# Kernel optimization log

Measured on AMD Instinct MI355X. Metric: run time of the kernel, lower is better.

## Reference

```python
import jax, jax.numpy as jnp
import numpy as np

N_NODES = 100000
N_EDGES = 1600000
F_IN, F_HID, F_OUT = 256, 128, 32


def setup_inputs() -> dict:
    key = jax.random.key(0)
    k1, k2, k3, k4 = jax.random.split(key, 4)
    x = jax.random.normal(k1, (N_NODES, F_IN), dtype=jnp.float32)
    edge_index = jax.random.randint(k2, (2, N_EDGES), 0, N_NODES, dtype=jnp.int64)
    W1 = jax.random.normal(k3, (F_IN, F_HID), dtype=jnp.float32) * (1.0 / np.sqrt(F_IN))
    b1 = jnp.zeros((F_HID,), dtype=jnp.float32)
    W2 = jax.random.normal(k4, (F_HID, F_OUT), dtype=jnp.float32) * (1.0 / np.sqrt(F_HID))
    b2 = jnp.zeros((F_OUT,), dtype=jnp.float32)
    return {"x": x, "edge_index": edge_index, "W1": W1, "b1": b1, "W2": W2, "b2": b2}


def _gcn_norm(edge_index, num_nodes):
    # Add self-loops, then symmetric normalization deg^-1/2[src] * deg^-1/2[dst].
    loops = jnp.arange(num_nodes, dtype=edge_index.dtype)
    src = jnp.concatenate([edge_index[0], loops])
    dst = jnp.concatenate([edge_index[1], loops])
    deg = jax.ops.segment_sum(jnp.ones_like(dst, dtype=jnp.float32), dst,
                              num_segments=num_nodes)
    dinv = jnp.where(deg > 0, jax.lax.rsqrt(deg), 0.0)
    norm = dinv[src] * dinv[dst]  # [E + N]
    return src, dst, norm


def _gcn_conv(h, src, dst, norm, num_nodes):
    # h already linearly transformed. Gather sources, scale, scatter-add to dst.
    msgs = h[src] * norm[:, None]
    return jax.ops.segment_sum(msgs, dst, num_segments=num_nodes)


def reference(x, edge_index, W1, b1, W2, b2):
    n = x.shape[0]
    src, dst, norm = _gcn_norm(edge_index, n)
    # Layer 1: linear -> normalized scatter-add -> bias -> relu
    h = _gcn_conv(x @ W1, src, dst, norm, n) + b1
    h = jax.nn.relu(h)
    # F.dropout with training=False (eval mode) is identity.
    # Layer 2
    out = _gcn_conv(h @ W2, src, dst, norm, n) + b2
    return jax.nn.log_softmax(out, axis=1)
```

## Files before the change

### kernel.cpp

```cpp
#include <hip/hip_runtime.h>

#define N_NODES 100000
#define N_EDGES 1600000
#define F_IN 256
#define F_HID 128
#define F_OUT 32
#define NBUCK 391
#define BIN_BLOCKS 512
#define EDGES_PER_BIN 3125

typedef unsigned short ushort_t;
typedef unsigned int uint_t;

using short8  = __attribute__((ext_vector_type(8))) short;
using floatx4 = __attribute__((ext_vector_type(4))) float;

__device__ __forceinline__ ushort_t f2bf(float f) {
    uint_t u = __float_as_uint(f);
    u += 0x7fff + ((u >> 16) & 1);
    return (ushort_t)(u >> 16);
}
__device__ __forceinline__ float bf_lo(uint_t u) { return __uint_as_float(u << 16); }
__device__ __forceinline__ float bf_hi(uint_t u) { return __uint_as_float(u & 0xffff0000u); }

__global__ __launch_bounds__(256) void hist_kernel(const int* __restrict__ ei,
                                                   int* __restrict__ bucket_cnt) {
    __shared__ int h[NBUCK];
    for (int i = threadIdx.x; i < NBUCK; i += 256) h[i] = 0;
    __syncthreads();
    int gid = blockIdx.x * 256 + threadIdx.x;
    for (int e = gid; e < N_EDGES; e += BIN_BLOCKS * 256)
        atomicAdd(&h[ei[N_EDGES + e] >> 8], 1);
    __syncthreads();
    for (int i = threadIdx.x; i < NBUCK; i += 256) {
        int c = h[i];
        if (c) atomicAdd(&bucket_cnt[i], c);
    }
}

__global__ __launch_bounds__(512) void scan_kernel(const int* __restrict__ bucket_cnt,
                                                   int* __restrict__ bucket_base,
                                                   int* __restrict__ bucket_cursor,
                                                   int* __restrict__ offs) {
    __shared__ int s[512];
    int t = threadIdx.x;
    int own = (t < NBUCK) ? bucket_cnt[t] : 0;
    s[t] = own;
    __syncthreads();
    for (int off = 1; off < 512; off <<= 1) {
        int v = (t >= off) ? s[t - off] : 0;
        __syncthreads();
        s[t] += v;
        __syncthreads();
    }
    if (t < NBUCK) {
        int ex = s[t] - own;
        bucket_base[t] = ex;
        bucket_cursor[t] = ex;
    }
    if (t == 0) {
        bucket_base[NBUCK] = N_EDGES;
        offs[N_NODES] = N_EDGES;
    }
}

__global__ __launch_bounds__(256) void bin_kernel(const int* __restrict__ ei,
                                                  int* __restrict__ bucket_cursor,
                                                  int2* __restrict__ binned) {
    __shared__ int h[NBUCK];
    __shared__ int base[NBUCK];
    const int t = threadIdx.x;
    const int beg = blockIdx.x * EDGES_PER_BIN;
    const int end = beg + EDGES_PER_BIN;
    for (int i = t; i < NBUCK; i += 256) h[i] = 0;
    __syncthreads();
    for (int e = beg + t; e < end; e += 256) atomicAdd(&h[ei[N_EDGES + e] >> 8], 1);
    __syncthreads();
    for (int i = t; i < NBUCK; i += 256) {
        int c = h[i];
        base[i] = c ? atomicAdd(&bucket_cursor[i], c) : 0;
        h[i] = 0;
    }
    __syncthreads();
    for (int e = beg + t; e < end; e += 256) {
        int s = ei[e], d = ei[N_EDGES + e];
        int bk = d >> 8;
        int p = base[bk] + atomicAdd(&h[bk], 1);
        binned[p] = make_int2(s, d);
    }
}

__global__ __launch_bounds__(256) void build_kernel(const int2* __restrict__ binned,
                                                    const int* __restrict__ bucket_base,
                                                    int* __restrict__ offs,
                                                    int* __restrict__ csr,
                                                    float* __restrict__ dinv) {
    __shared__ int h[256];
    __shared__ int sc[256];
    __shared__ int cur[256];
    const int b = blockIdx.x, t = threadIdx.x;
    const int beg = bucket_base[b];
    const int end = bucket_base[b + 1];
    h[t] = 0;
    __syncthreads();
    for (int j = beg + t; j < end; j += 256) {
        int2 p = binned[j];
        atomicAdd(&h[p.y & 255], 1);
    }
    __syncthreads();
    int deg = h[t];
    sc[t] = deg;
    __syncthreads();
    for (int off = 1; off < 256; off <<= 1) {
        int v = (t >= off) ? sc[t - off] : 0;
        __syncthreads();
        sc[t] += v;
        __syncthreads();
    }
    int excl = sc[t] - deg;
    cur[t] = excl;
    int node = b * 256 + t;
    if (node < N_NODES) {
        offs[node] = beg + excl;
        dinv[node] = rsqrtf((float)deg + 1.0f);
    }
    __syncthreads();
    for (int j = beg + t; j < end; j += 256) {
        int2 p = binned[j];
        int pos = atomicAdd(&cur[p.y & 255], 1);
        csr[beg + pos] = p.x;
    }
}

__global__ __launch_bounds__(256) void w1t_kernel(const float* __restrict__ W1,
                                                  ushort_t* __restrict__ W1T) {
    int t = blockIdx.x * 256 + threadIdx.x;
#pragma unroll
    for (int j = 0; j < 4; j++) {
        int e = j * 8192 + t;
        int n = e >> 8, k = e & 255;
        W1T[e] = f2bf(W1[k * F_HID + n]);
    }
}

__global__ __launch_bounds__(256) void gemm1_kernel(const float* __restrict__ x,
                                                    const ushort_t* __restrict__ W1T,
                                                    ushort_t* __restrict__ h0bf) {
    __shared__ ushort_t Bst[F_HID][F_IN + 8];
    const int tid = threadIdx.x;
    const int rbase = blockIdx.x * 64;
    const int w = tid >> 6;
    const int lane = tid & 63;
    const int q = lane >> 4;
    const int nloc = lane & 15;

#pragma unroll
    for (int j = 0; j < 16; j++) {
        int f = j * 256 + tid;
        int n = f >> 5, kg = f & 31;
        uint4 v = ((const uint4*)(W1T + n * F_IN))[kg];
        *(uint4*)(&Bst[n][kg * 8]) = v;
    }
    __syncthreads();

    const int rowA = rbase + w * 16 + nloc;
    const bool okA = rowA < N_NODES;
    const float* ap = x + (size_t)rowA * F_IN + q * 8;

    floatx4 acc[8];
#pragma unroll
    for (int t = 0; t < 8; t++) acc[t] = (floatx4){0.f, 0.f, 0.f, 0.f};

#pragma unroll
    for (int k0 = 0; k0 < F_IN; k0 += 32) {
        float4 f0 = make_float4(0.f, 0.f, 0.f, 0.f);
        float4 f1 = make_float4(0.f, 0.f, 0.f, 0.f);
        if (okA) {
            f0 = *(const float4*)(ap + k0);
            f1 = *(const float4*)(ap + k0 + 4);
        }
        short8 a;
        a[0] = (short)f2bf(f0.x); a[1] = (short)f2bf(f0.y);
        a[2] = (short)f2bf(f0.z); a[3] = (short)f2bf(f0.w);
        a[4] = (short)f2bf(f1.x); a[5] = (short)f2bf(f1.y);
        a[6] = (short)f2bf(f1.z); a[7] = (short)f2bf(f1.w);
#pragma unroll
        for (int t = 0; t < 8; t++) {
            short8 b = *(const short8*)(&Bst[t * 16 + nloc][k0 + q * 8]);
            acc[t] = __builtin_amdgcn_mfma_f32_16x16x32_bf16(a, b, acc[t], 0, 0, 0);
        }
    }

#pragma unroll
    for (int reg = 0; reg < 4; reg++) {
        int rowD = rbase + w * 16 + q * 4 + reg;
        if (rowD < N_NODES) {
            ushort_t* op = h0bf + (size_t)rowD * F_HID + nloc;
#pragma unroll
            for (int t = 0; t < 8; t++) op[t * 16] = f2bf(acc[t][reg]);
        }
    }
}

__global__ __launch_bounds__(256) void gather128(const ushort_t* __restrict__ h0bf,
                                                 const int* __restrict__ offs,
                                                 const int* __restrict__ csr,
                                                 const float* __restrict__ dinv,
                                                 ushort_t* __restrict__ aggbf) {
    int node = blockIdx.x * 8 + (threadIdx.x >> 5);
    int l = threadIdx.x & 31;
    float dn = dinv[node];
    uint2 sv = ((const uint2*)(h0bf + (size_t)node * F_HID))[l];
    float s = dn * dn;
    float4 acc;
    acc.x = bf_lo(sv.x) * s; acc.y = bf_hi(sv.x) * s;
    acc.z = bf_lo(sv.y) * s; acc.w = bf_hi(sv.y) * s;

    int beg = offs[node], end = offs[node + 1];
    int j = beg;
    for (; j + 1 < end; j += 2) {
        int s0 = csr[j], s1 = csr[j + 1];
        float n0 = dinv[s0] * dn, n1 = dinv[s1] * dn;
        uint2 v0 = ((const uint2*)(h0bf + (size_t)s0 * F_HID))[l];
        uint2 v1 = ((const uint2*)(h0bf + (size_t)s1 * F_HID))[l];
        acc.x += bf_lo(v0.x) * n0 + bf_lo(v1.x) * n1;
        acc.y += bf_hi(v0.x) * n0 + bf_hi(v1.x) * n1;
        acc.z += bf_lo(v0.y) * n0 + bf_lo(v1.y) * n1;
        acc.w += bf_hi(v0.y) * n0 + bf_hi(v1.y) * n1;
    }
    if (j < end) {
        int s0 = csr[j];
        float n0 = dinv[s0] * dn;
        uint2 v0 = ((const uint2*)(h0bf + (size_t)s0 * F_HID))[l];
        acc.x += bf_lo(v0.x) * n0; acc.y += bf_hi(v0.x) * n0;
        acc.z += bf_lo(v0.y) * n0; acc.w += bf_hi(v0.y) * n0;
    }
    uint2 p;
    p.x = (uint_t)f2bf(acc.x) | ((uint_t)f2bf(acc.y) << 16);
    p.y = (uint_t)f2bf(acc.z) | ((uint_t)f2bf(acc.w) << 16);
    ((uint2*)(aggbf + (size_t)node * F_HID))[l] = p;
}

__global__ __launch_bounds__(256) void gemm2_kernel(const ushort_t* __restrict__ aggbf,
                                                    const float* __restrict__ b1,
                                                    const float* __restrict__ W2,
                                                    ushort_t* __restrict__ h2bf) {
    __shared__ float Ws[F_HID * F_OUT];
    __shared__ float As[64][F_HID + 1];
    __shared__ float b1s[F_HID];
    const int tid = threadIdx.x;
    const int rbase = blockIdx.x * 64;

    if (tid < F_HID) b1s[tid] = b1[tid];
#pragma unroll
    for (int j = 0; j < 4; j++) {
        int f = tid + 256 * j;
        ((float4*)Ws)[f] = ((const float4*)W2)[f];
    }
    __syncthreads();

#pragma unroll
    for (int j = 0; j < 4; j++) {
        int f = tid + 256 * j;
        int row = f >> 4, u4 = f & 15;
        int gr = rbase + row;
        uint4 v = make_uint4(0, 0, 0, 0);
        if (gr < N_NODES) v = ((const uint4*)(aggbf + (size_t)gr * F_HID))[u4];
        int c = u4 * 8;
        As[row][c + 0] = fmaxf(bf_lo(v.x) + b1s[c + 0], 0.f);
        As[row][c + 1] = fmaxf(bf_hi(v.x) + b1s[c + 1], 0.f);
        As[row][c + 2] = fmaxf(bf_lo(v.y) + b1s[c + 2], 0.f);
        As[row][c + 3] = fmaxf(bf_hi(v.y) + b1s[c + 3], 0.f);
        As[row][c + 4] = fmaxf(bf_lo(v.z) + b1s[c + 4], 0.f);
        As[row][c + 5] = fmaxf(bf_hi(v.z) + b1s[c + 5], 0.f);
        As[row][c + 6] = fmaxf(bf_lo(v.w) + b1s[c + 6], 0.f);
        As[row][c + 7] = fmaxf(bf_hi(v.w) + b1s[c + 7], 0.f);
    }
    __syncthreads();

    const int r = tid >> 2;
    const int c0 = (tid & 3) * 8;
    float acc[8] = {0, 0, 0, 0, 0, 0, 0, 0};
#pragma unroll 4
    for (int k = 0; k < F_HID; k++) {
        float a = As[r][k];
#pragma unroll
        for (int j = 0; j < 8; j++) acc[j] += a * Ws[k * F_OUT + c0 + j];
    }
    int gr = rbase + r;
    if (gr < N_NODES) {
        uint4 p;
        p.x = (uint_t)f2bf(acc[0]) | ((uint_t)f2bf(acc[1]) << 16);
        p.y = (uint_t)f2bf(acc[2]) | ((uint_t)f2bf(acc[3]) << 16);
        p.z = (uint_t)f2bf(acc[4]) | ((uint_t)f2bf(acc[5]) << 16);
        p.w = (uint_t)f2bf(acc[6]) | ((uint_t)f2bf(acc[7]) << 16);
        *(uint4*)(h2bf + (size_t)gr * F_OUT + c0) = p;
    }
}

__global__ __launch_bounds__(256) void gather32_lsm(const ushort_t* __restrict__ h2bf,
                                                    const int* __restrict__ offs,
                                                    const int* __restrict__ csr,
                                                    const float* __restrict__ dinv,
                                                    const float* __restrict__ b2,
                                                    float* __restrict__ out) {
    int node = blockIdx.x * 32 + (threadIdx.x >> 3);
    int l = threadIdx.x & 7;
    float dn = dinv[node];
    uint2 sv = ((const uint2*)(h2bf + (size_t)node * F_OUT))[l];
    float s = dn * dn;
    float4 acc;
    acc.x = bf_lo(sv.x) * s; acc.y = bf_hi(sv.x) * s;
    acc.z = bf_lo(sv.y) * s; acc.w = bf_hi(sv.y) * s;

    int beg = offs[node], end = offs[node + 1];
    int j = beg;
    for (; j + 1 < end; j += 2) {
        int s0 = csr[j], s1 = csr[j + 1];
        float n0 = dinv[s0] * dn, n1 = dinv[s1] * dn;
        uint2 v0 = ((const uint2*)(h2bf + (size_t)s0 * F_OUT))[l];
        uint2 v1 = ((const uint2*)(h2bf + (size_t)s1 * F_OUT))[l];
        acc.x += bf_lo(v0.x) * n0 + bf_lo(v1.x) * n1;
        acc.y += bf_hi(v0.x) * n0 + bf_hi(v1.x) * n1;
        acc.z += bf_lo(v0.y) * n0 + bf_lo(v1.y) * n1;
        acc.w += bf_hi(v0.y) * n0 + bf_hi(v1.y) * n1;
    }
    if (j < end) {
        int s0 = csr[j];
        float n0 = dinv[s0] * dn;
        uint2 v0 = ((const uint2*)(h2bf + (size_t)s0 * F_OUT))[l];
        acc.x += bf_lo(v0.x) * n0; acc.y += bf_hi(v0.x) * n0;
        acc.z += bf_lo(v0.y) * n0; acc.w += bf_hi(v0.y) * n0;
    }
    float4 bb = ((const float4*)b2)[l];
    acc.x += bb.x; acc.y += bb.y; acc.z += bb.z; acc.w += bb.w;

    float m = fmaxf(fmaxf(acc.x, acc.y), fmaxf(acc.z, acc.w));
#pragma unroll
    for (int off = 1; off < 8; off <<= 1) m = fmaxf(m, __shfl_xor(m, off, 8));
    float es = __expf(acc.x - m) + __expf(acc.y - m) + __expf(acc.z - m) + __expf(acc.w - m);
#pragma unroll
    for (int off = 1; off < 8; off <<= 1) es += __shfl_xor(es, off, 8);
    float lse = m + __logf(es);
    float4 o = make_float4(acc.x - lse, acc.y - lse, acc.z - lse, acc.w - lse);
    ((float4*)(out + (size_t)node * F_OUT))[l] = o;
}

extern "C" void kernel_launch(void* const* d_in, const int* in_sizes, int n_in,
                              void* d_out, int out_size, void* d_ws, size_t ws_size,
                              hipStream_t stream) {
    const float* x  = (const float*)d_in[0];
    const int*   ei = (const int*)d_in[1];
    const float* W1 = (const float*)d_in[2];
    const float* b1 = (const float*)d_in[3];
    const float* W2 = (const float*)d_in[4];
    const float* b2 = (const float*)d_in[5];
    float* out = (float*)d_out;

    float* ws = (float*)d_ws;
    float*    dinv          = ws;
    int*      offs          = (int*)(ws + 100096);
    int*      bucket_cnt    = (int*)(ws + 200224);
    int*      bucket_base   = (int*)(ws + 200736);
    int*      bucket_cursor = (int*)(ws + 201248);
    int*      csr           = (int*)(ws + 201760);
    ushort_t* W1T           = (ushort_t*)(ws + 1801760);
    ushort_t* h0bf          = (ushort_t*)(ws + 1818144);
    ushort_t* aggbf         = (ushort_t*)(ws + 8218144);
    ushort_t* h2bf          = (ushort_t*)(ws + 14618144);
    int2*     binned        = (int2*)aggbf;

    hipMemsetAsync(bucket_cnt, 0, 512 * sizeof(int), stream);
    hist_kernel<<<BIN_BLOCKS, 256, 0, stream>>>(ei, bucket_cnt);
    scan_kernel<<<1, 512, 0, stream>>>(bucket_cnt, bucket_base, bucket_cursor, offs);
    bin_kernel<<<BIN_BLOCKS, 256, 0, stream>>>(ei, bucket_cursor, binned);
    build_kernel<<<NBUCK, 256, 0, stream>>>(binned, bucket_base, offs, csr, dinv);
    w1t_kernel<<<32, 256, 0, stream>>>(W1, W1T);
    gemm1_kernel<<<(N_NODES + 63) / 64, 256, 0, stream>>>(x, W1T, h0bf);
    gather128<<<N_NODES / 8, 256, 0, stream>>>(h0bf, offs, csr, dinv, aggbf);
    gemm2_kernel<<<(N_NODES + 63) / 64, 256, 0, stream>>>(aggbf, b1, W2, h2bf);
    gather32_lsm<<<N_NODES / 32, 256, 0, stream>>>(h2bf, offs, csr, dinv, b2, out);
}
```

Baseline: 400.5 us.

## Use bf16 MFMA for second GEMM and unroll gathers by four edges

Rewrites gemm2 to use the 16x16x32 bf16 MFMA instruction with a pre-transposed bf16 W2 staged in shared memory, replacing the scalar fp32 shared-memory GEMM. Bias and ReLU are applied in registers before the operands are packed to bf16. Both gather kernels now unroll the neighbour loop by four instead of two, so more independent row loads are in flight. The cost is one extra small transpose kernel launch and a bf16 rounding of the ReLU activations.

After: 361.0 us. 9.9% less time.

```diff
diff --git a/kernel.cpp b/kernel.cpp
--- a/kernel.cpp
+++ b/kernel.cpp
@@ -141,6 +141,13 @@
         int n = e >> 8, k = e & 255;
         W1T[e] = f2bf(W1[k * F_HID + n]);
     }
+}
+
+__global__ __launch_bounds__(256) void w2t_kernel(const float* __restrict__ W2,
+                                                  ushort_t* __restrict__ W2T) {
+    int e = blockIdx.x * 256 + threadIdx.x;
+    int n = e >> 7, k = e & 127;
+    W2T[e] = f2bf(W2[k * F_OUT + n]);
 }
 
 __global__ __launch_bounds__(256) void gemm1_kernel(const float* __restrict__ x,
@@ -218,17 +225,20 @@
 
     int beg = offs[node], end = offs[node + 1];
     int j = beg;
-    for (; j + 1 < end; j += 2) {
-        int s0 = csr[j], s1 = csr[j + 1];
+    for (; j + 3 < end; j += 4) {
+        int s0 = csr[j], s1 = csr[j + 1], s2 = csr[j + 2], s3 = csr[j + 3];
         float n0 = dinv[s0] * dn, n1 = dinv[s1] * dn;
+        float n2 = dinv[s2] * dn, n3 = dinv[s3] * dn;
         uint2 v0 = ((const uint2*)(h0bf + (size_t)s0 * F_HID))[l];
         uint2 v1 = ((const uint2*)(h0bf + (size_t)s1 * F_HID))[l];
-        acc.x += bf_lo(v0.x) * n0 + bf_lo(v1.x) * n1;
-        acc.y += bf_hi(v0.x) * n0 + bf_hi(v1.x) * n1;
-        acc.z += bf_lo(v0.y) * n0 + bf_lo(v1.y) * n1;
-        acc.w += bf_hi(v0.y) * n0 + bf_hi(v1.y) * n1;
-    }
-    if (j < end) {
+        uint2 v2 = ((const uint2*)(h0bf + (size_t)s2 * F_HID))[l];
+        uint2 v3 = ((const uint2*)(h0bf + (size_t)s3 * F_HID))[l];
+        acc.x += bf_lo(v0.x) * n0 + bf_lo(v1.x) * n1 + bf_lo(v2.x) * n2 + bf_lo(v3.x) * n3;
+        acc.y += bf_hi(v0.x) * n0 + bf_hi(v1.x) * n1 + bf_hi(v2.x) * n2 + bf_hi(v3.x) * n3;
+        acc.z += bf_lo(v0.y) * n0 + bf_lo(v1.y) * n1 + bf_lo(v2.y) * n2 + bf_lo(v3.y) * n3;
+        acc.w += bf_hi(v0.y) * n0 + bf_hi(v1.y) * n1 + bf_hi(v2.y) * n2 + bf_hi(v3.y) * n3;
+    }
+    for (; j < end; j++) {
         int s0 = csr[j];
         float n0 = dinv[s0] * dn;
         uint2 v0 = ((const uint2*)(h0bf + (size_t)s0 * F_HID))[l];
@@ -243,58 +253,64 @@
 
 __global__ __launch_bounds__(256) void gemm2_kernel(const ushort_t* __restrict__ aggbf,
                                                     const float* __restrict__ b1,
-                                                    const float* __restrict__ W2,
+                                                    const ushort_t* __restrict__ W2T,
                                                     ushort_t* __restrict__ h2bf) {
-    __shared__ float Ws[F_HID * F_OUT];
-    __shared__ float As[64][F_HID + 1];
+    __shared__ ushort_t Bs[F_OUT][F_HID + 8];
     __shared__ float b1s[F_HID];
     const int tid = threadIdx.x;
     const int rbase = blockIdx.x * 64;
+    const int w = tid >> 6;
+    const int lane = tid & 63;
+    const int q = lane >> 4;
+    const int nloc = lane & 15;
 
     if (tid < F_HID) b1s[tid] = b1[tid];
 #pragma unroll
-    for (int j = 0; j < 4; j++) {
-        int f = tid + 256 * j;
-        ((float4*)Ws)[f] = ((const float4*)W2)[f];
-    }
-    __syncthreads();
-
-#pragma unroll
-    for (int j = 0; j < 4; j++) {
-        int f = tid + 256 * j;
-        int row = f >> 4, u4 = f & 15;
-        int gr = rbase + row;
-        uint4 v = make_uint4(0, 0, 0, 0);
-        if (gr < N_NODES) v = ((const uint4*)(aggbf + (size_t)gr * F_HID))[u4];
-        int c = u4 * 8;
-        As[row][c + 0] = fmaxf(bf_lo(v.x) + b1s[c + 0], 0.f);
-        As[row][c + 1] = fmaxf(bf_hi(v.x) + b1s[c + 1], 0.f);
-        As[row][c + 2] = fmaxf(bf_lo(v.y) + b1s[c + 2], 0.f);
-        As[row][c + 3] = fmaxf(bf_hi(v.y) + b1s[c + 3], 0.f);
-        As[row][c + 4] = fmaxf(bf_lo(v.z) + b1s[c + 4], 0.f);
-        As[row][c + 5] = fmaxf(bf_hi(v.z) + b1s[c + 5], 0.f);
-        As[row][c + 6] = fmaxf(bf_lo(v.w) + b1s[c + 6], 0.f);
-        As[row][c + 7] = fmaxf(bf_hi(v.w) + b1s[c + 7], 0.f);
-    }
-    __syncthreads();
-
-    const int r = tid >> 2;
-    const int c0 = (tid & 3) * 8;
-    float acc[8] = {0, 0, 0, 0, 0, 0, 0, 0};
-#pragma unroll 4
-    for (int k = 0; k < F_HID; k++) {
-        float a = As[r][k];
-#pragma unroll
-        for (int j = 0; j < 8; j++) acc[j] += a * Ws[k * F_OUT + c0 + j];
-    }
-    int gr = rbase + r;
-    if (gr < N_NODES) {
-        uint4 p;
-        p.x = (uint_t)f2bf(acc[0]) | ((uint_t)f2bf(acc[1]) << 16);
-        p.y = (uint_t)f2bf(acc[2]) | ((uint_t)f2bf(acc[3]) << 16);
-        p.z = (uint_t)f2bf(acc[4]) | ((uint_t)f2bf(acc[5]) << 16);
-        p.w = (uint_t)f2bf(acc[6]) | ((uint_t)f2bf(acc[7]) << 16);
-        *(uint4*)(h2bf + (size_t)gr * F_OUT + c0) = p;
+    for (int jj = 0; jj < 2; jj++) {
+        int f = jj * 256 + tid;
+        int n = f >> 4, kg = f & 15;
+        uint4 v = ((const uint4*)(W2T + n * F_HID))[kg];
+        *(uint4*)(&Bs[n][kg * 8]) = v;
+    }
+    __syncthreads();
+
+    const int rowA = rbase + w * 16 + nloc;
+    const bool okA = rowA < N_NODES;
+
+    floatx4 acc[2];
+    acc[0] = (floatx4){0.f, 0.f, 0.f, 0.f};
+    acc[1] = (floatx4){0.f, 0.f, 0.f, 0.f};
+
+#pragma unroll
+    for (int k0 = 0; k0 < F_HID; k0 += 32) {
+        int kk = k0 + q * 8;
+        uint4 av = make_uint4(0, 0, 0, 0);
+        if (okA) av = *(const uint4*)(aggbf + (size_t)rowA * F_HID + kk);
+        float4 bb0 = *(const float4*)(&b1s[kk]);
+        float4 bb1 = *(const float4*)(&b1s[kk + 4]);
+        short8 a;
+        a[0] = (short)f2bf(fmaxf(bf_lo(av.x) + bb0.x, 0.f));
+        a[1] = (short)f2bf(fmaxf(bf_hi(av.x) + bb0.y, 0.f));
+        a[2] = (short)f2bf(fmaxf(bf_lo(av.y) + bb0.z, 0.f));
+        a[3] = (short)f2bf(fmaxf(bf_hi(av.y) + bb0.w, 0.f));
+        a[4] = (short)f2bf(fmaxf(bf_lo(av.z) + bb1.x, 0.f));
+        a[5] = (short)f2bf(fmaxf(bf_hi(av.z) + bb1.y, 0.f));
+        a[6] = (short)f2bf(fmaxf(bf_lo(av.w) + bb1.z, 0.f));
+        a[7] = (short)f2bf(fmaxf(bf_hi(av.w) + bb1.w, 0.f));
+#pragma unroll
+        for (int t = 0; t < 2; t++) {
+            short8 b = *(const short8*)(&Bs[t * 16 + nloc][kk]);
+            acc[t] = __builtin_amdgcn_mfma_f32_16x16x32_bf16(a, b, acc[t], 0, 0, 0);
+        }
+    }
+#pragma unroll
+    for (int reg = 0; reg < 4; reg++) {
+        int rowD = rbase + w * 16 + q * 4 + reg;
+        if (rowD < N_NODES) {
+            ushort_t* op = h2bf + (size_t)rowD * F_OUT + nloc;
+            op[0]  = f2bf(acc[0][reg]);
+            op[16] = f2bf(acc[1][reg]);
+        }
     }
 }
 
@@ -315,17 +331,20 @@
 
     int beg = offs[node], end = offs[node + 1];
     int j = beg;
-    for (; j + 1 < end; j += 2) {
-        int s0 = csr[j], s1 = csr[j + 1];
+    for (; j + 3 < end; j += 4) {
+        int s0 = csr[j], s1 = csr[j + 1], s2 = csr[j + 2], s3 = csr[j + 3];
         float n0 = dinv[s0] * dn, n1 = dinv[s1] * dn;
+        float n2 = dinv[s2] * dn, n3 = dinv[s3] * dn;
         uint2 v0 = ((const uint2*)(h2bf + (size_t)s0 * F_OUT))[l];
         uint2 v1 = ((const uint2*)(h2bf + (size_t)s1 * F_OUT))[l];
-        acc.x += bf_lo(v0.x) * n0 + bf_lo(v1.x) * n1;
-        acc.y += bf_hi(v0.x) * n0 + bf_hi(v1.x) * n1;
-        acc.z += bf_lo(v0.y) * n0 + bf_lo(v1.y) * n1;
-        acc.w += bf_hi(v0.y) * n0 + bf_hi(v1.y) * n1;
-    }
-    if (j < end) {
+        uint2 v2 = ((const uint2*)(h2bf + (size_t)s2 * F_OUT))[l];
+        uint2 v3 = ((const uint2*)(h2bf + (size_t)s3 * F_OUT))[l];
+        acc.x += bf_lo(v0.x) * n0 + bf_lo(v1.x) * n1 + bf_lo(v2.x) * n2 + bf_lo(v3.x) * n3;
+        acc.y += bf_hi(v0.x) * n0 + bf_hi(v1.x) * n1 + bf_hi(v2.x) * n2 + bf_hi(v3.x) * n3;
+        acc.z += bf_lo(v0.y) * n0 + bf_lo(v1.y) * n1 + bf_lo(v2.y) * n2 + bf_lo(v3.y) * n3;
+        acc.w += bf_hi(v0.y) * n0 + bf_hi(v1.y) * n1 + bf_hi(v2.y) * n2 + bf_hi(v3.y) * n3;
+    }
+    for (; j < end; j++) {
         int s0 = csr[j];
         float n0 = dinv[s0] * dn;
         uint2 v0 = ((const uint2*)(h2bf + (size_t)s0 * F_OUT))[l];
@@ -365,9 +384,10 @@
     int*      bucket_cursor = (int*)(ws + 201248);
     int*      csr           = (int*)(ws + 201760);
     ushort_t* W1T           = (ushort_t*)(ws + 1801760);
-    ushort_t* h0bf          = (ushort_t*)(ws + 1818144);
-    ushort_t* aggbf         = (ushort_t*)(ws + 8218144);
-    ushort_t* h2bf          = (ushort_t*)(ws + 14618144);
+    ushort_t* W2T           = (ushort_t*)(ws + 1818144);
+    ushort_t* h0bf          = (ushort_t*)(ws + 1820192);
+    ushort_t* aggbf         = (ushort_t*)(ws + 8220192);
+    ushort_t* h2bf          = (ushort_t*)(ws + 14620192);
     int2*     binned        = (int2*)aggbf;
 
     hipMemsetAsync(bucket_cnt, 0, 512 * sizeof(int), stream);
@@ -376,8 +396,9 @@
     bin_kernel<<<BIN_BLOCKS, 256, 0, stream>>>(ei, bucket_cursor, binned);
     build_kernel<<<NBUCK, 256, 0, stream>>>(binned, bucket_base, offs, csr, dinv);
     w1t_kernel<<<32, 256, 0, stream>>>(W1, W1T);
+    w2t_kernel<<<16, 256, 0, stream>>>(W2, W2T);
     gemm1_kernel<<<(N_NODES + 63) / 64, 256, 0, stream>>>(x, W1T, h0bf);
     gather128<<<N_NODES / 8, 256, 0, stream>>>(h0bf, offs, csr, dinv, aggbf);
-    gemm2_kernel<<<(N_NODES + 63) / 64, 256, 0, stream>>>(aggbf, b1, W2, h2bf);
+    gemm2_kernel<<<(N_NODES + 63) / 64, 256, 0, stream>>>(aggbf, b1, W2T, h2bf);
     gather32_lsm<<<N_NODES / 32, 256, 0, stream>>>(h2bf, offs, csr, dinv, b2, out);
 }
```
